# Kernel tuning notes

Hardware: AMD Instinct MI355X
Metric: run time of the kernel (lower is better)

The kernel has to match this reference:

```python
import jax, jax.numpy as jnp
import numpy as np

POOL = 7  # fixed 7x7 output grid, hard-coded in the original layer


def _bin_bounds(step, rlen):
    # Replicates the original bin-corner logic + empty-bin adjustment.
    i = jnp.arange(POOL, dtype=jnp.int32)
    s = i * step
    e = jnp.where(i < POOL - 1, (i + 1) * step, rlen)
    empty = s == e
    # original: grow end by 1 if room, else shrink start by 1
    e = jnp.where(empty & (e < rlen), e + 1, e)
    s = jnp.where(empty & ~(e > (i * step)) , s, s)  # no-op placeholder for clarity
    s = jnp.where(empty & ((i * step) == e), (i * step) - 1, jnp.where(empty, i * step, s))
    # simpler equivalent: if still empty after trying to grow end, shrink start
    s0 = i * step
    e0 = jnp.where(i < POOL - 1, (i + 1) * step, rlen)
    grow = empty & (e0 < rlen)
    e = jnp.where(grow, e0 + 1, e0)
    s = jnp.where(empty & ~grow, s0 - 1, s0)
    return s, e


def _pool_one(roi, fm):
    # fm: [H, W, C]; roi: [4] normalized (y1, x1, y2, x2)
    H, W, C = fm.shape
    h0 = (H * roi[0]).astype(jnp.int32)  # tf.cast to int32 truncates (floor for >=0)
    w0 = (W * roi[1]).astype(jnp.int32)
    h1 = (H * roi[2]).astype(jnp.int32)
    w1 = (W * roi[3]).astype(jnp.int32)
    rh = h1 - h0
    rw = w1 - w0
    hstep = rh // POOL
    wstep = rw // POOL
    sh, eh = _bin_bounds(hstep, rh)  # [7], region-relative
    sw, ew = _bin_bounds(wstep, rw)
    hidx = jnp.arange(H, dtype=jnp.int32)
    widx = jnp.arange(W, dtype=jnp.int32)
    rmask = (hidx[None, :] >= (h0 + sh)[:, None]) & (hidx[None, :] < (h0 + eh)[:, None])  # [7,H]
    cmask = (widx[None, :] >= (w0 + sw)[:, None]) & (widx[None, :] < (w0 + ew)[:, None])  # [7,W]
    neg = jnp.asarray(-jnp.inf, fm.dtype)
    # max over rows for each of the 7 row-bins: [7, W, C]
    t = jnp.max(jnp.where(rmask[:, :, None, None], fm[None, :, :, :], neg), axis=1)
    # max over cols for each of the 7 col-bins: [7, 7, C]
    out = jnp.max(jnp.where(cmask[None, :, :, None], t[:, None, :, :], neg), axis=2)
    return out


def setup_inputs() -> dict:
    key = jax.random.key(0)
    k_f, k_y, k_x, k_h, k_w = jax.random.split(key, 5)
    H, W, C, N = 50, 50, 1024, 300
    features = jax.random.normal(k_f, (1, H, W, C), dtype=jnp.float32)
    # well-formed normalized ROIs: y1 < y2, x1 < x2, extent in [0.2, 0.55]
    y1 = jax.random.uniform(k_y, (N,), minval=0.0, maxval=0.45)
    x1 = jax.random.uniform(k_x, (N,), minval=0.0, maxval=0.45)
    hh = jax.random.uniform(k_h, (N,), minval=0.2, maxval=0.55)
    ww = jax.random.uniform(k_w, (N,), minval=0.2, maxval=0.55)
    rois = jnp.stack([y1, x1, jnp.minimum(y1 + hh, 1.0), jnp.minimum(x1 + ww, 1.0)], axis=1).astype(jnp.float32)
    return {"features": features, "rois": rois}


def reference(features, rois):
    fm = jnp.squeeze(features, axis=0)  # [H, W, C]
    # sequential over ROIs (mirrors tf.while_loop), fully vectorized per ROI
    pooled = jax.lax.map(lambda r: _pool_one(r, fm), rois)  # [N, 7, 7, C]
    return pooled
```

## Files before the change

### kernel.cpp

```cpp
#include <hip/hip_runtime.h>
#include <math.h>

#define POOL 7
#define FH 50
#define FW 50
#define FC 1024
#define FC4 (FC / 4)
#define CHUNKS 4
#define F4C 64

typedef float vf4 __attribute__((ext_vector_type(4)));

static __device__ __forceinline__ vf4 vmax4(vf4 a, vf4 b) {
    vf4 r;
    r.x = fmaxf(a.x, b.x);
    r.y = fmaxf(a.y, b.y);
    r.z = fmaxf(a.z, b.z);
    r.w = fmaxf(a.w, b.w);
    return r;
}

__global__ __launch_bounds__(256) void roipool_kernel(
    const float* __restrict__ fm,
    const float* __restrict__ rois,
    float* __restrict__ out,
    int nbins)
{
    const int b     = blockIdx.x;
    const int chunk = b & (CHUNKS - 1);
    const int wave  = threadIdx.x >> 6;
    const int lane  = threadIdx.x & 63;
    const int gid   = (b >> 2) * 4 + wave;
    if (gid >= nbins) return;

    const int n  = gid / 49;
    const int ij = gid - n * 49;
    const int i  = ij / 7;
    const int j  = ij - i * 7;

    const float4 roi = reinterpret_cast<const float4*>(rois)[n];
    const int h0 = (int)((float)FH * roi.x);
    const int w0 = (int)((float)FW * roi.y);
    const int h1 = (int)((float)FH * roi.z);
    const int w1 = (int)((float)FW * roi.w);
    const int rh = h1 - h0;
    const int rw = w1 - w0;
    const int hstep = rh / POOL;
    const int wstep = rw / POOL;

    int sh = i * hstep;
    int eh = (i < POOL - 1) ? (i + 1) * hstep : rh;
    if (sh == eh) { if (eh < rh) eh += 1; else sh -= 1; }
    int sw = j * wstep;
    int ew = (j < POOL - 1) ? (j + 1) * wstep : rw;
    if (sw == ew) { if (ew < rw) ew += 1; else sw -= 1; }

    const int r0 = max(0, h0 + sh);
    const int r1 = min(FH, h0 + eh);
    const int c0 = max(0, w0 + sw);
    const int c1 = min(FW, w0 + ew);

    const int f4 = chunk * F4C + lane;

    vf4 acc = {-INFINITY, -INFINITY, -INFINITY, -INFINITY};

    const vf4* fm4 = reinterpret_cast<const vf4*>(fm);

    for (int r = r0; r < r1; ++r) {
        const vf4* rowp = fm4 + (size_t)(r * FW) * FC4 + f4;
        int c = c0;
        for (; c + 1 < c1; c += 2) {
            vf4 a = rowp[(size_t)c * FC4];
            vf4 b2 = rowp[(size_t)(c + 1) * FC4];
            acc = vmax4(acc, vmax4(a, b2));
        }
        if (c < c1) {
            acc = vmax4(acc, rowp[(size_t)c * FC4]);
        }
    }

    vf4* o = reinterpret_cast<vf4*>(out) + (size_t)gid * FC4 + f4;
    __builtin_nontemporal_store(acc, o);
}

extern "C" void kernel_launch(void* const* d_in, const int* in_sizes, int n_in,
                              void* d_out, int out_size, void* d_ws, size_t ws_size,
                              hipStream_t stream) {
    const float* features = (const float*)d_in[0];
    const float* rois     = (const float*)d_in[1];
    float* out            = (float*)d_out;
    const int N = in_sizes[1] / 4;

    const int nbins = N * POOL * POOL;
    dim3 grid(((nbins + 3) / 4) * CHUNKS);
    dim3 block(256);
    roipool_kernel<<<grid, block, 0, stream>>>(features, rois, out, nbins);
}
```

Measured before the change: 98.72 us.

## Process a full row of seven bins per wave instead of one bin

Each wave now handles one ROI and one row-bin and computes all seven column bins with seven accumulators, so ROI decoding and bin-bound math are shared across them. The grid shrinks by a factor of seven, which cuts the total wave count. In exchange each wave carries more serial work and registers, and there are fewer waves to hide memory latency on a workload that reads heavily from L2. Column bins do not overlap, so the total feature reads stay roughly the same.

```diff
diff --git a/kernel.cpp b/kernel.cpp
--- a/kernel.cpp
+++ b/kernel.cpp
@@ -8,6 +8,7 @@
 #define FC4 (FC / 4)
 #define CHUNKS 4
 #define F4C 64
+#define ROWSTRIDE (FW * FC4)
 
 typedef float vf4 __attribute__((ext_vector_type(4)));
 
@@ -24,19 +25,17 @@
     const float* __restrict__ fm,
     const float* __restrict__ rois,
     float* __restrict__ out,
-    int nbins)
+    int nunits)
 {
     const int b     = blockIdx.x;
     const int chunk = b & (CHUNKS - 1);
     const int wave  = threadIdx.x >> 6;
     const int lane  = threadIdx.x & 63;
-    const int gid   = (b >> 2) * 4 + wave;
-    if (gid >= nbins) return;
+    const int unit  = (b >> 2) * 4 + wave;
+    if (unit >= nunits) return;
 
-    const int n  = gid / 49;
-    const int ij = gid - n * 49;
-    const int i  = ij / 7;
-    const int j  = ij - i * 7;
+    const int n = unit / POOL;
+    const int i = unit - n * POOL;
 
     const float4 roi = reinterpret_cast<const float4*>(rois)[n];
     const int h0 = (int)((float)FH * roi.x);
@@ -51,36 +50,51 @@
     int sh = i * hstep;
     int eh = (i < POOL - 1) ? (i + 1) * hstep : rh;
     if (sh == eh) { if (eh < rh) eh += 1; else sh -= 1; }
-    int sw = j * wstep;
-    int ew = (j < POOL - 1) ? (j + 1) * wstep : rw;
-    if (sw == ew) { if (ew < rw) ew += 1; else sw -= 1; }
-
     const int r0 = max(0, h0 + sh);
     const int r1 = min(FH, h0 + eh);
-    const int c0 = max(0, w0 + sw);
-    const int c1 = min(FW, w0 + ew);
+
+    int c0[POOL], c1[POOL];
+#pragma unroll
+    for (int j = 0; j < POOL; ++j) {
+        int sw = j * wstep;
+        int ew = (j < POOL - 1) ? (j + 1) * wstep : rw;
+        if (sw == ew) { if (ew < rw) ew += 1; else sw -= 1; }
+        c0[j] = max(0, w0 + sw);
+        c1[j] = min(FW, w0 + ew);
+    }
 
     const int f4 = chunk * F4C + lane;
+    const vf4* fmbase = reinterpret_cast<const vf4*>(fm) + f4;
 
-    vf4 acc = {-INFINITY, -INFINITY, -INFINITY, -INFINITY};
-
-    const vf4* fm4 = reinterpret_cast<const vf4*>(fm);
+    vf4 acc[POOL];
+#pragma unroll
+    for (int j = 0; j < POOL; ++j) {
+        acc[j].x = -INFINITY; acc[j].y = -INFINITY;
+        acc[j].z = -INFINITY; acc[j].w = -INFINITY;
+    }
 
     for (int r = r0; r < r1; ++r) {
-        const vf4* rowp = fm4 + (size_t)(r * FW) * FC4 + f4;
-        int c = c0;
-        for (; c + 1 < c1; c += 2) {
-            vf4 a = rowp[(size_t)c * FC4];
-            vf4 b2 = rowp[(size_t)(c + 1) * FC4];
-            acc = vmax4(acc, vmax4(a, b2));
-        }
-        if (c < c1) {
-            acc = vmax4(acc, rowp[(size_t)c * FC4]);
+        const vf4* rowp = fmbase + r * ROWSTRIDE;
+#pragma unroll
+        for (int j = 0; j < POOL; ++j) {
+            int c = c0[j];
+            const int ce = c1[j];
+            for (; c + 1 < ce; c += 2) {
+                vf4 a  = rowp[c * FC4];
+                vf4 b2 = rowp[(c + 1) * FC4];
+                acc[j] = vmax4(acc[j], vmax4(a, b2));
+            }
+            if (c < ce) {
+                acc[j] = vmax4(acc[j], rowp[c * FC4]);
+            }
         }
     }
 
-    vf4* o = reinterpret_cast<vf4*>(out) + (size_t)gid * FC4 + f4;
-    __builtin_nontemporal_store(acc, o);
+    vf4* o = reinterpret_cast<vf4*>(out) + (size_t)(n * 49 + i * 7) * FC4 + f4;
+#pragma unroll
+    for (int j = 0; j < POOL; ++j) {
+        __builtin_nontemporal_store(acc[j], o + (size_t)j * FC4);
+    }
 }
 
 extern "C" void kernel_launch(void* const* d_in, const int* in_sizes, int n_in,
@@ -91,8 +105,8 @@
     float* out            = (float*)d_out;
     const int N = in_sizes[1] / 4;
 
-    const int nbins = N * POOL * POOL;
-    dim3 grid(((nbins + 3) / 4) * CHUNKS);
+    const int nunits = N * POOL;
+    dim3 grid(((nunits + 3) / 4) * CHUNKS);
     dim3 block(256);
-    roipool_kernel<<<grid, block, 0, stream>>>(features, rois, out, nbins);
+    roipool_kernel<<<grid, block, 0, stream>>>(features, rois, out, nunits);
 }
```

New measurement: 117.3 us. +18.8%, slower.

## Stage per-channel-group feature slab in LDS and pool all bins from it

Applied to the files above, without the earlier changes.

Each block now loads an 8-channel slice of the whole 50x50 feature map into shared memory once, padded with stride 3 to spread LDS accesses. Its threads then compute every ROI bin (split across 2 blocks) for that slice by reading LDS, where before each wave re-read overlapping global rows per bin. This removes the redundant global and L2 traffic from overlapping ROIs. In exchange the grid drops to 256 blocks of 512 threads, each writing scattered 32-byte output pieces, and a 120 KB LDS allocation limits occupancy to one block per CU.

```diff
diff --git a/kernel.cpp b/kernel.cpp
--- a/kernel.cpp
+++ b/kernel.cpp
@@ -5,9 +5,13 @@
 #define FH 50
 #define FW 50
 #define FC 1024
-#define FC4 (FC / 4)
-#define CHUNKS 4
-#define F4C 64
+#define NCELLS (FH * FW)
+#define CH_PER_BLOCK 8
+#define CHG4 2
+#define LDS_STRIDE 3
+#define CH_GROUPS (FC / CH_PER_BLOCK)
+#define NSPLIT 2
+#define THREADS 512
 
 typedef float vf4 __attribute__((ext_vector_type(4)));
 
@@ -20,67 +24,82 @@
     return r;
 }
 
-__global__ __launch_bounds__(256) void roipool_kernel(
+__global__ __launch_bounds__(THREADS, 1) void roipool_lds_kernel(
     const float* __restrict__ fm,
     const float* __restrict__ rois,
     float* __restrict__ out,
-    int nbins)
+    int nrois)
 {
+    __shared__ vf4 lds4[NCELLS * LDS_STRIDE];
+
     const int b     = blockIdx.x;
-    const int chunk = b & (CHUNKS - 1);
-    const int wave  = threadIdx.x >> 6;
-    const int lane  = threadIdx.x & 63;
-    const int gid   = (b >> 2) * 4 + wave;
-    if (gid >= nbins) return;
+    const int chgrp = b & (CH_GROUPS - 1);
+    const int split = b >> 7;
+    const int c0ch  = chgrp * CH_PER_BLOCK;
 
-    const int n  = gid / 49;
-    const int ij = gid - n * 49;
-    const int i  = ij / 7;
-    const int j  = ij - i * 7;
+    for (int m = threadIdx.x; m < NCELLS * CHG4; m += THREADS) {
+        const int cell = m >> 1;
+        const int g    = m & 1;
+        const vf4 v = *reinterpret_cast<const vf4*>(
+            fm + (size_t)cell * FC + c0ch + g * 4);
+        lds4[cell * LDS_STRIDE + g] = v;
+    }
+    __syncthreads();
 
-    const float4 roi = reinterpret_cast<const float4*>(rois)[n];
-    const int h0 = (int)((float)FH * roi.x);
-    const int w0 = (int)((float)FW * roi.y);
-    const int h1 = (int)((float)FH * roi.z);
-    const int w1 = (int)((float)FW * roi.w);
-    const int rh = h1 - h0;
-    const int rw = w1 - w0;
-    const int hstep = rh / POOL;
-    const int wstep = rw / POOL;
+    const int btot = nrois * POOL * POOL;
+    const int per  = (btot + NSPLIT - 1) / NSPLIT;
+    const int bq0  = split * per;
+    const int bq1  = (bq0 + per < btot) ? (bq0 + per) : btot;
+    const int nout = (bq1 - bq0) * CHG4;
 
-    int sh = i * hstep;
-    int eh = (i < POOL - 1) ? (i + 1) * hstep : rh;
-    if (sh == eh) { if (eh < rh) eh += 1; else sh -= 1; }
-    int sw = j * wstep;
-    int ew = (j < POOL - 1) ? (j + 1) * wstep : rw;
-    if (sw == ew) { if (ew < rw) ew += 1; else sw -= 1; }
+    for (int k = threadIdx.x; k < nout; k += THREADS) {
+        const int bl  = k >> 1;
+        const int g   = k & 1;
+        const int bin = bq0 + bl;
+        const int n   = bin / 49;
+        const int ij  = bin - n * 49;
+        const int i   = ij / 7;
+        const int j   = ij - i * 7;
 
-    const int r0 = max(0, h0 + sh);
-    const int r1 = min(FH, h0 + eh);
-    const int c0 = max(0, w0 + sw);
-    const int c1 = min(FW, w0 + ew);
+        const float4 roi = reinterpret_cast<const float4*>(rois)[n];
+        const int h0 = (int)((float)FH * roi.x);
+        const int w0 = (int)((float)FW * roi.y);
+        const int h1 = (int)((float)FH * roi.z);
+        const int w1 = (int)((float)FW * roi.w);
+        const int rh = h1 - h0;
+        const int rw = w1 - w0;
+        const int hstep = rh / POOL;
+        const int wstep = rw / POOL;
 
-    const int f4 = chunk * F4C + lane;
+        int sh = i * hstep;
+        int eh = (i < POOL - 1) ? (i + 1) * hstep : rh;
+        if (sh == eh) { if (eh < rh) eh += 1; else sh -= 1; }
+        int sw = j * wstep;
+        int ew = (j < POOL - 1) ? (j + 1) * wstep : rw;
+        if (sw == ew) { if (ew < rw) ew += 1; else sw -= 1; }
+        const int r0 = max(0, h0 + sh);
+        const int r1 = min(FH, h0 + eh);
+        const int cA = max(0, w0 + sw);
+        const int cB = min(FW, w0 + ew);
 
-    vf4 acc = {-INFINITY, -INFINITY, -INFINITY, -INFINITY};
+        vf4 acc = {-INFINITY, -INFINITY, -INFINITY, -INFINITY};
+        for (int r = r0; r < r1; ++r) {
+            const int rowc = r * FW;
+            vf4 acc2 = {-INFINITY, -INFINITY, -INFINITY, -INFINITY};
+            int c = cA;
+            for (; c + 1 < cB; c += 2) {
+                acc  = vmax4(acc,  lds4[(rowc + c)     * LDS_STRIDE + g]);
+                acc2 = vmax4(acc2, lds4[(rowc + c + 1) * LDS_STRIDE + g]);
+            }
+            if (c < cB) {
+                acc = vmax4(acc, lds4[(rowc + c) * LDS_STRIDE + g]);
+            }
+            acc = vmax4(acc, acc2);
+        }
 
-    const vf4* fm4 = reinterpret_cast<const vf4*>(fm);
-
-    for (int r = r0; r < r1; ++r) {
-        const vf4* rowp = fm4 + (size_t)(r * FW) * FC4 + f4;
-        int c = c0;
-        for (; c + 1 < c1; c += 2) {
-            vf4 a = rowp[(size_t)c * FC4];
-            vf4 b2 = rowp[(size_t)(c + 1) * FC4];
-            acc = vmax4(acc, vmax4(a, b2));
-        }
-        if (c < c1) {
-            acc = vmax4(acc, rowp[(size_t)c * FC4]);
-        }
+        vf4* o = reinterpret_cast<vf4*>(out + (size_t)bin * FC + c0ch) + g;
+        __builtin_nontemporal_store(acc, o);
     }
-
-    vf4* o = reinterpret_cast<vf4*>(out) + (size_t)gid * FC4 + f4;
-    __builtin_nontemporal_store(acc, o);
 }
 
 extern "C" void kernel_launch(void* const* d_in, const int* in_sizes, int n_in,
@@ -91,8 +110,7 @@
     float* out            = (float*)d_out;
     const int N = in_sizes[1] / 4;
 
-    const int nbins = N * POOL * POOL;
-    dim3 grid(((nbins + 3) / 4) * CHUNKS);
-    dim3 block(256);
-    roipool_kernel<<<grid, block, 0, stream>>>(features, rois, out, nbins);
+    dim3 grid(CH_GROUPS * NSPLIT);
+    dim3 block(THREADS);
+    roipool_lds_kernel<<<grid, block, 0, stream>>>(features, rois, out, N);
 }
```

After: 149.3 us. 1.51x slower.
